# Kernel tuning notes

Hardware: AMD Instinct MI355X
Metric: run time of the kernel (lower is better)

## Reference

```python
import jax, jax.numpy as jnp
import numpy as np

N, E, B = 50000, 800000, 64
IN_DIM, HID = 128, 64
H1 = 2  # heads in gat1
NEG_SLOPE = 0.2


def _glorot(key, shape):
    fan_in = shape[0]
    return jax.random.normal(key, shape, dtype=jnp.float32) / jnp.sqrt(jnp.float32(fan_in))


def setup_inputs() -> dict:
    key = jax.random.key(0)
    ks = jax.random.split(key, 24)
    x = jax.random.normal(ks[0], (N, IN_DIM), dtype=jnp.float32)
    edge_index = jax.random.randint(ks[1], (2, E), 0, N, dtype=jnp.int64)
    batch = jnp.sort(jax.random.randint(ks[2], (N,), 0, B, dtype=jnp.int64))
    d = {
        'x': x, 'edge_index': edge_index, 'batch': batch,
        # gat1: in=128 -> heads=2, out=64 (concat -> 128)
        'w1_l': _glorot(ks[3], (IN_DIM, H1 * HID)), 'b1_l': jnp.zeros((H1 * HID,), jnp.float32),
        'w1_r': _glorot(ks[4], (IN_DIM, H1 * HID)), 'b1_r': jnp.zeros((H1 * HID,), jnp.float32),
        'att1': _glorot(ks[5], (H1, HID)), 'bias1': jnp.zeros((H1 * HID,), jnp.float32),
        # gat2: in=128 -> heads=1, out=64
        'w2_l': _glorot(ks[6], (H1 * HID, HID)), 'b2_l': jnp.zeros((HID,), jnp.float32),
        'w2_r': _glorot(ks[7], (H1 * HID, HID)), 'b2_r': jnp.zeros((HID,), jnp.float32),
        'att2': _glorot(ks[8], (1, HID)), 'bias2': jnp.zeros((HID,), jnp.float32),
        # gate_nn: Linear(64,64) -> ReLU -> Linear(64,1)
        'gate_w1': _glorot(ks[9], (HID, HID)), 'gate_b1': jnp.zeros((HID,), jnp.float32),
        'gate_w2': _glorot(ks[10], (HID, 1)), 'gate_b2': jnp.zeros((1,), jnp.float32),
        # MLP head
        'lin1_w': _glorot(ks[11], (HID, HID)), 'lin1_b': jnp.zeros((HID,), jnp.float32),
        'lin2_w': _glorot(ks[12], (HID, 1)), 'lin2_b': jnp.zeros((1,), jnp.float32),
    }
    return d


def _segment_softmax(scores, seg, num_segments):
    # scores: [E, H]; softmax over edges sharing the same seg id (per column)
    m = jax.ops.segment_max(scores, seg, num_segments=num_segments)
    m = jnp.where(jnp.isfinite(m), m, 0.0)
    ex = jnp.exp(scores - m[seg])
    s = jax.ops.segment_sum(ex, seg, num_segments=num_segments)
    return ex / (s[seg] + 1e-16)


def _gatv2(x, src, dst, w_l, b_l, w_r, b_r, att, bias, heads, out_dim, n_nodes):
    xl = (x @ w_l + b_l).reshape(n_nodes, heads, out_dim)
    xr = (x @ w_r + b_r).reshape(n_nodes, heads, out_dim)
    e = jax.nn.leaky_relu(xl[src] + xr[dst], NEG_SLOPE)      # [E,H,D]
    score = jnp.einsum('ehd,hd->eh', e, att)                  # [E,H]
    alpha = _segment_softmax(score, dst, n_nodes)             # [E,H]
    out = jax.ops.segment_sum(alpha[..., None] * xl[src], dst, num_segments=n_nodes)
    return out.reshape(n_nodes, heads * out_dim) + bias


def reference(x, edge_index, batch, w1_l, b1_l, w1_r, b1_r, att1, bias1,
              w2_l, b2_l, w2_r, b2_r, att2, bias2,
              gate_w1, gate_b1, gate_w2, gate_b2,
              lin1_w, lin1_b, lin2_w, lin2_b):
    n = x.shape[0]
    # PyG GATv2Conv default add_self_loops=True
    loop = jnp.arange(n, dtype=edge_index.dtype)
    src = jnp.concatenate([edge_index[0], loop])
    dst = jnp.concatenate([edge_index[1], loop])

    h = jax.nn.relu(_gatv2(x, src, dst, w1_l, b1_l, w1_r, b1_r, att1, bias1, H1, HID, n))
    h = jax.nn.relu(_gatv2(h, src, dst, w2_l, b2_l, w2_r, b2_r, att2, bias2, 1, HID, n))

    # GlobalAttention pool: gate = gate_nn(h); softmax over batch; weighted sum
    gate = jax.nn.relu(h @ gate_w1 + gate_b1) @ gate_w2 + gate_b2     # [N,1]
    alpha = _segment_softmax(gate, batch, B)                           # [N,1]
    pooled = jax.ops.segment_sum(alpha * h, batch, num_segments=B)     # [B,HID]

    out = jax.nn.relu(pooled @ lin1_w + lin1_b)
    out = (out @ lin2_w + lin2_b).squeeze(-1)                          # [B]
    return out
```

## Files before the change

kernel.cpp:

```cpp
#include <hip/hip_runtime.h>

typedef float v2f __attribute__((ext_vector_type(2)));
typedef float v4f __attribute__((ext_vector_type(4)));
typedef _Float16 h4 __attribute__((ext_vector_type(4)));
typedef _Float16 f16x8 __attribute__((ext_vector_type(8)));

template<int N> struct IC { static constexpr int value = N; };


__global__ void k_init(const float* __restrict__ w1_l, const float* __restrict__ w1_r,
                       const float* __restrict__ b1_l, const float* __restrict__ b1_r,
                       const float* __restrict__ w2_l, const float* __restrict__ w2_r,
                       const float* __restrict__ b2_l, const float* __restrict__ b2_r,
                       _Float16* __restrict__ wc1h, _Float16* __restrict__ wc1l,
                       _Float16* __restrict__ wc2h, _Float16* __restrict__ wc2l,
                       float* __restrict__ bc1, float* __restrict__ bc2,
                       int* __restrict__ deg, int n){
  int i = blockIdx.x*256 + threadIdx.x;
  if (i < n) deg[i] = 0;
  if (i < 256*128){
    int col = i >> 7, k = i & 127;
    float v = (col < 128) ? w1_l[k*128 + col] : w1_r[k*128 + (col - 128)];
    _Float16 h = (_Float16)v;
    wc1h[i] = h; wc1l[i] = (_Float16)(v - (float)h);
  }
  if (i < 128*128){
    int col = i >> 7, k = i & 127;
    float v = (col < 64) ? w2_l[k*64 + col] : w2_r[k*64 + (col - 64)];
    _Float16 h = (_Float16)v;
    wc2h[i] = h; wc2l[i] = (_Float16)(v - (float)h);
  }
  if (i < 256) bc1[i] = (i < 128) ? b1_l[i] : b1_r[i - 128];
  if (i < 128) bc2[i] = (i < 64)  ? b2_l[i] : b2_r[i - 64];
}

#define SCB 256

__global__ __launch_bounds__(256) void k_hist_xcd(
    const int* __restrict__ dstp, int* __restrict__ deg, int E, int n){
  int b = blockIdx.x;
  int reg = b & 7;
  int chunk = b >> 3;
  int lo = (int)((long long)reg * n >> 3);
  int hi = (int)((long long)(reg + 1) * n >> 3);
  int per = (E + SCB - 1) / SCB;
  int e0 = chunk * per;
  int e1 = min(E, e0 + per);
  for (int e = e0 + threadIdx.x; e < e1; e += 256){
    int d = dstp[e];
    if (d >= lo && d < hi) atomicAdd(&deg[d], 1);
  }
}

__global__ void k_scan1(const int* __restrict__ deg, int* __restrict__ rowptr,
                        int* __restrict__ bsum, int n){
  __shared__ int s[256];
  int i = blockIdx.x*256 + threadIdx.x;
  int v = (i < n) ? deg[i] + 1 : 0;
  s[threadIdx.x] = v;
  __syncthreads();
  for (int off = 1; off < 256; off <<= 1){
    int t = (threadIdx.x >= off) ? s[threadIdx.x - off] : 0;
    __syncthreads();
    s[threadIdx.x] += t;
    __syncthreads();
  }
  if (i < n) rowptr[i] = s[threadIdx.x] - v;
  if (threadIdx.x == 255) bsum[blockIdx.x] = s[255];
}

__global__ void k_scan2(int* bsum, int nb){
  __shared__ int s[256];
  int v = (threadIdx.x < nb) ? bsum[threadIdx.x] : 0;
  s[threadIdx.x] = v;
  __syncthreads();
  for (int off = 1; off < 256; off <<= 1){
    int t = (threadIdx.x >= off) ? s[threadIdx.x - off] : 0;
    __syncthreads();
    s[threadIdx.x] += t;
    __syncthreads();
  }
  if (threadIdx.x < nb) bsum[threadIdx.x] = s[threadIdx.x] - v;
}

__global__ void k_scan3(int* rowptr, const int* __restrict__ bsum,
                        int* __restrict__ srcs, int* __restrict__ cursor,
                        int n, int total){
  int i = blockIdx.x*256 + threadIdx.x;
  if (i < n){
    int b = rowptr[i] + bsum[blockIdx.x];
    rowptr[i] = b;
    srcs[b] = i;
    cursor[i] = b + 1;
  }
  if (i == 0) rowptr[n] = total;
}

__global__ __launch_bounds__(256) void k_scatter_xcd(
    const int* __restrict__ srcp, const int* __restrict__ dstp,
    int* __restrict__ cursor, int* __restrict__ srcs, int E, int n){
  int b = blockIdx.x;
  int reg = b & 7;
  int chunk = b >> 3;
  int lo = (int)((long long)reg * n >> 3);
  int hi = (int)((long long)(reg + 1) * n >> 3);
  int per = (E + SCB - 1) / SCB;
  int e0 = chunk * per;
  int e1 = min(E, e0 + per);
  for (int e = e0 + threadIdx.x; e < e1; e += 256){
    int d = dstp[e];
    if (d >= lo && d < hi){
      int p = atomicAdd(&cursor[d], 1);
      srcs[p] = srcp[e];
    }
  }
}


#define MBM 64
#define MBN 128
#define MBK 32

__device__ __forceinline__ int lds_idx(int row, int k){
  return row*32 + ((((k >> 3) ^ row) & 3) << 3) + (k & 7);
}

__global__ __launch_bounds__(256) void k_gemm_mfma(
    const float* __restrict__ A, const _Float16* __restrict__ Wh,
    const _Float16* __restrict__ Wl, const float* __restrict__ bias,
    _Float16* __restrict__ Cxl, float* __restrict__ Cxr,
    int M, int K, int N, int xlCols){
  __shared__ _Float16 Ah[MBM*MBK], Al[MBM*MBK];
  __shared__ _Float16 Bh[MBN*MBK], Bl[MBN*MBK];
  int bm = blockIdx.x * MBM, bn = blockIdx.y * MBN;
  int tid = threadIdx.x;
  int lane = tid & 63, wv = tid >> 6;
  v4f acc[8] = {};
  const int fragoff = (lane & 15)*32 + ((((lane >> 4) ^ lane) & 3) << 3);
  for (int k0 = 0; k0 < K; k0 += MBK){
    #pragma unroll
    for (int l = 0; l < 2; l++){
      int idx = tid + l*256;
      int r = idx >> 3, kq = (idx & 7) * 4;
      float4 v = make_float4(0.f, 0.f, 0.f, 0.f);
      if (bm + r < M) v = *(const float4*)(A + (size_t)(bm + r)*K + k0 + kq);
      _Float16 e0 = (_Float16)v.x, e1 = (_Float16)v.y,
               e2 = (_Float16)v.z, e3 = (_Float16)v.w;
      h4 hh = {e0, e1, e2, e3};
      h4 ll = {(_Float16)(v.x - (float)e0), (_Float16)(v.y - (float)e1),
               (_Float16)(v.z - (float)e2), (_Float16)(v.w - (float)e3)};
      int o = lds_idx(r, kq);
      *(h4*)(&Ah[o]) = hh;
      *(h4*)(&Al[o]) = ll;
    }
    #pragma unroll
    for (int l = 0; l < 2; l++){
      int idx = tid + l*256;
      int c = idx >> 2, kc = (idx & 3) * 8;
      size_t go = (size_t)(bn + c)*K + k0 + kc;
      int o = lds_idx(c, kc);
      *(f16x8*)(&Bh[o]) = *(const f16x8*)(Wh + go);
      *(f16x8*)(&Bl[o]) = *(const f16x8*)(Wl + go);
    }
    __syncthreads();
    f16x8 ah = *(const f16x8*)(&Ah[wv*16*32 + fragoff]);
    f16x8 al = *(const f16x8*)(&Al[wv*16*32 + fragoff]);
    #pragma unroll
    for (int t = 0; t < 8; t++){
      f16x8 bh = *(const f16x8*)(&Bh[t*16*32 + fragoff]);
      f16x8 bl = *(const f16x8*)(&Bl[t*16*32 + fragoff]);
      acc[t] = __builtin_amdgcn_mfma_f32_16x16x32_f16(ah, bh, acc[t], 0, 0, 0);
      acc[t] = __builtin_amdgcn_mfma_f32_16x16x32_f16(ah, bl, acc[t], 0, 0, 0);
      acc[t] = __builtin_amdgcn_mfma_f32_16x16x32_f16(al, bh, acc[t], 0, 0, 0);
    }
    __syncthreads();
  }
  int rbase = bm + wv*16 + (lane >> 4)*4;
  int cl = lane & 15;
  int NR = N - xlCols;
  #pragma unroll
  for (int t = 0; t < 8; t++){
    int col = bn + t*16 + cl;
    float bv = bias[col];
    bool isXl = (bn + t*16) < xlCols;
    #pragma unroll
    for (int i = 0; i < 4; i++){
      int r = rbase + i;
      if (r < M){
        float o = acc[t][i] + bv;
        if (isXl) Cxl[(size_t)r*xlCols + col] = (_Float16)o;
        else      Cxr[(size_t)r*NR + (col - xlCols)] = o;
      }
    }
  }
}


template<int CTRL>
__device__ __forceinline__ float dpp_add(float x){
  int t = __builtin_amdgcn_update_dpp(0, __float_as_int(x), CTRL, 0xf, 0xf, true);
  return x + __int_as_float(t);
}


template<int H>
__global__ __launch_bounds__(128) void k_gat_fused(
    const _Float16* __restrict__ xlh, const float* __restrict__ xr,
    const int* __restrict__ rowptr, const int* __restrict__ srcs,
    const float* __restrict__ att, const float* __restrict__ bias,
    float* __restrict__ out, int n){
  int gid = blockIdx.x * blockDim.x + threadIdx.x;
  int nd = gid >> 6, lane = gid & 63;
  if (nd >= n) return;
  constexpr int SHIFTB = (H == 2) ? 8 : 7;
  constexpr int EPI = (H == 2) ? 2 : 4;
  const int q = lane & 15;
  const int hsel = (H == 2) ? ((lane >> 4) & 1) : 0;
  const int elane = (H == 2) ? (lane >> 5) : (lane >> 4);
  const int fpos = hsel*64 + q*4;
  const unsigned foff = (unsigned)fpos * 2u;
  const char* __restrict__ xbase = (const char*)xlh;
  v4f xrv = *(const v4f*)(xr + (size_t)nd*(H*64) + fpos);
  v4f av  = *(const v4f*)(att + fpos);
  v4f acc = {0.f, 0.f, 0.f, 0.f};
  float den = 0.f;
  int s0 = rowptr[nd], s1 = rowptr[nd+1];
  for (int base = s0; base < s1; base += 64){
    int idx = base + lane;
    int sv = (idx < s1) ? srcs[idx] : 0;
    int cnt = min(64, s1 - base);
    auto batchU = [&](int i, auto Uc, bool full){
      constexpr int U = decltype(Uc)::value;
      int aidx[U];
      h4 hv[U];
      #pragma unroll
      for (int u = 0; u < U; u++)
        aidx[u] = __builtin_amdgcn_ds_bpermute((i + u*EPI + elane) << 2, sv);
      #pragma unroll
      for (int u = 0; u < U; u++)
        hv[u] = *(const h4*)(xbase + (((unsigned)aidx[u] << SHIFTB) + foff));
      #pragma unroll
      for (int u = 0; u < U; u++){
        v4f xv = {(float)hv[u].x, (float)hv[u].y, (float)hv[u].z, (float)hv[u].w};
        v4f t  = xv + xrv;
        v4f lt = __builtin_elementwise_max(t, t * 0.2f);
        v4f pr = lt * av;
        float p = (pr.x + pr.y) + (pr.z + pr.w);
        p = dpp_add<0x111>(p);
        p = dpp_add<0x112>(p);
        p = dpp_add<0x114>(p);
        p = dpp_add<0x118>(p);
        p = __int_as_float(__builtin_amdgcn_ds_swizzle(__float_as_int(p), 0x1F0));
        float ex = __expf(p);
        if (!full) ex = (elane < cnt - (i + u*EPI)) ? ex : 0.f;
        den += ex;
        acc += xv * ex;
      }
    };
    int i = 0;
    for (; i + 8*EPI <= cnt; i += 8*EPI) batchU(i, IC<8>{}, true);
    if (i + 4*EPI <= cnt){ batchU(i, IC<4>{}, true); i += 4*EPI; }
    if (i + 2*EPI <= cnt){ batchU(i, IC<2>{}, true); i += 2*EPI; }
    for (; i < cnt; i += EPI) batchU(i, IC<1>{}, i + EPI <= cnt);
  }
  if (H == 1){
    den   += __shfl_xor(den,   16, 64);
    acc.x += __shfl_xor(acc.x, 16, 64);
    acc.y += __shfl_xor(acc.y, 16, 64);
    acc.z += __shfl_xor(acc.z, 16, 64);
    acc.w += __shfl_xor(acc.w, 16, 64);
  }
  den   += __shfl_xor(den,   32, 64);
  acc.x += __shfl_xor(acc.x, 32, 64);
  acc.y += __shfl_xor(acc.y, 32, 64);
  acc.z += __shfl_xor(acc.z, 32, 64);
  acc.w += __shfl_xor(acc.w, 32, 64);
  if (lane < 16*H){
    v4f bv = *(const v4f*)(bias + fpos);
    float inv = 1.f / (den + 1e-16f);
    v4f o = acc * inv + bv;
    v4f z = {0.f, 0.f, 0.f, 0.f};
    o = __builtin_elementwise_max(o, z);
    *(v4f*)(out + (size_t)nd*(H*64) + fpos) = o;
  }
}


__global__ __launch_bounds__(256) void k_gate(
    const float* __restrict__ h2, const float* __restrict__ gw1,
    const float* __restrict__ gb1, const float* __restrict__ gw2,
    const float* __restrict__ gb2, float* __restrict__ exn, int M){
  __shared__ float As[32][64 + 4];
  __shared__ float Ws[32][64];
  int bm = blockIdx.x * 64;
  int tid = threadIdx.x;
  int tx = tid & 15, ty = tid >> 4;
  float acc[4][4] = {};
  for (int k0 = 0; k0 < 64; k0 += 32){
    #pragma unroll
    for (int l = 0; l < 2; l++){
      int idx = tid + l*256;
      int r = idx >> 3, c4 = (idx & 7) * 4;
      float4 v = make_float4(0.f, 0.f, 0.f, 0.f);
      if (bm + r < M) v = *(const float4*)(h2 + (size_t)(bm + r)*64 + k0 + c4);
      As[c4+0][r] = v.x; As[c4+1][r] = v.y; As[c4+2][r] = v.z; As[c4+3][r] = v.w;
      int kr = idx >> 4, wc4 = (idx & 15) * 4;
      *(float4*)(&Ws[kr][wc4]) = *(const float4*)(gw1 + (size_t)(k0 + kr)*64 + wc4);
    }
    __syncthreads();
    #pragma unroll
    for (int k = 0; k < 32; k++){
      float4 a4 = *(const float4*)(&As[k][ty*4]);
      float4 w4 = *(const float4*)(&Ws[k][tx*4]);
      float av[4] = {a4.x, a4.y, a4.z, a4.w};
      float wv[4] = {w4.x, w4.y, w4.z, w4.w};
      #pragma unroll
      for (int i = 0; i < 4; i++)
        #pragma unroll
        for (int j = 0; j < 4; j++)
          acc[i][j] = fmaf(av[i], wv[j], acc[i][j]);
    }
    __syncthreads();
  }
  float4 b4 = *(const float4*)(gb1 + tx*4);
  float4 w2 = *(const float4*)(gw2 + tx*4);
  float gb2v = gb2[0];
  #pragma unroll
  for (int i = 0; i < 4; i++){
    float p = fmaxf(acc[i][0] + b4.x, 0.f) * w2.x;
    p = fmaf(fmaxf(acc[i][1] + b4.y, 0.f), w2.y, p);
    p = fmaf(fmaxf(acc[i][2] + b4.z, 0.f), w2.z, p);
    p = fmaf(fmaxf(acc[i][3] + b4.w, 0.f), w2.w, p);
    p = dpp_add<0x111>(p);
    p = dpp_add<0x112>(p);
    p = dpp_add<0x114>(p);
    p = dpp_add<0x118>(p);
    if (tx == 15){
      int r = bm + ty*4 + i;
      if (r < M) exn[r] = __expf(p + gb2v);
    }
  }
}


__global__ __launch_bounds__(1024) void k_pool_mlp(
    const float* __restrict__ h2, const float* __restrict__ exn,
    const int* __restrict__ batch, int n,
    const float* __restrict__ l1w, const float* __restrict__ l1b,
    const float* __restrict__ l2w, const float* __restrict__ l2b,
    float* __restrict__ out){
  __shared__ float accs[16][64];
  __shared__ float dens[16];
  int b = blockIdx.x;
  int tid = threadIdx.x, lane = tid & 63, wv = tid >> 6;
  int lo = 0, hi = n;
  while (lo < hi){ int m = (lo + hi) >> 1; if (batch[m] < b) lo = m + 1; else hi = m; }
  int start = lo;
  hi = n;
  while (lo < hi){ int m = (lo + hi) >> 1; if (batch[m] < b + 1) lo = m + 1; else hi = m; }
  int end = lo;
  float acc = 0.f, den = 0.f;
  for (int nd = start + wv; nd < end; nd += 16){
    float ex = exn[nd];
    den += ex;
    acc = fmaf(ex, h2[(size_t)nd*64 + lane], acc);
  }
  accs[wv][lane] = acc;
  if (lane == 0) dens[wv] = den;
  __syncthreads();
  if (wv == 0){
    float p = 0.f, d = 0.f;
    #pragma unroll
    for (int w = 0; w < 16; w++){ p += accs[w][lane]; d += dens[w]; }
    p = p / (d + 1e-16f);
    float t = l1b[lane];
    #pragma unroll
    for (int k = 0; k < 64; k++)
      t = fmaf(__shfl(p, k, 64), l1w[k*64 + lane], t);
    t = fmaxf(t, 0.f) * l2w[lane];
    #pragma unroll
    for (int off = 32; off; off >>= 1) t += __shfl_xor(t, off, 64);
    if (lane == 0) out[b] = t + l2b[0];
  }
}


extern "C" void kernel_launch(void* const* d_in, const int* in_sizes, int n_in,
                              void* d_out, int out_size, void* d_ws, size_t ws_size,
                              hipStream_t stream){
  const float* x    = (const float*)d_in[0];
  const int*   ei   = (const int*)  d_in[1];
  const int*   batch= (const int*)  d_in[2];
  const float* w1_l = (const float*)d_in[3];  const float* b1_l = (const float*)d_in[4];
  const float* w1_r = (const float*)d_in[5];  const float* b1_r = (const float*)d_in[6];
  const float* att1 = (const float*)d_in[7];  const float* bias1= (const float*)d_in[8];
  const float* w2_l = (const float*)d_in[9];  const float* b2_l = (const float*)d_in[10];
  const float* w2_r = (const float*)d_in[11]; const float* b2_r = (const float*)d_in[12];
  const float* att2 = (const float*)d_in[13]; const float* bias2= (const float*)d_in[14];
  const float* gw1  = (const float*)d_in[15]; const float* gb1  = (const float*)d_in[16];
  const float* gw2  = (const float*)d_in[17]; const float* gb2  = (const float*)d_in[18];
  const float* l1w  = (const float*)d_in[19]; const float* l1b  = (const float*)d_in[20];
  const float* l2w  = (const float*)d_in[21]; const float* l2b  = (const float*)d_in[22];

  const int n = in_sizes[0] / 128;
  const int E = in_sizes[1] / 2;
  const int Bb = out_size;
  const int Etot = E + n;
  const int* srcp = ei;
  const int* dstp = ei + E;

  char* wsbase = (char*)d_ws;
  size_t off = 0;
  auto alloc = [&](size_t bytes)->char*{
    char* p = wsbase + off;
    off = (off + bytes + 255) & ~(size_t)255;
    return p;
  };
  int*   deg    = (int*)  alloc((size_t)n*4);
  int*   rowptr = (int*)  alloc((size_t)(n+1)*4);
  int*   cursor = (int*)  alloc((size_t)n*4);
  int*   bsum   = (int*)  alloc(1024);
  int*   srcs   = (int*)  alloc((size_t)Etot*4);
  _Float16* wc1h = (_Float16*)alloc(256*128*2);
  _Float16* wc1l = (_Float16*)alloc(256*128*2);
  _Float16* wc2h = (_Float16*)alloc(128*128*2);
  _Float16* wc2l = (_Float16*)alloc(128*128*2);
  float* bc1    = (float*)alloc(256*4);
  float* bc2    = (float*)alloc(128*4);
  _Float16* xlh1 = (_Float16*)alloc((size_t)n*128*2);
  float* xr1    = (float*)alloc((size_t)n*128*4);
  float* h1     = (float*)alloc((size_t)n*128*4);
  _Float16* xlh2 = xlh1;
  float* xr2 = xr1;
  float* h2  = xr1 + (size_t)n*64;
  float* exn = h1;

  int nb = (n + 255) / 256;
  int ib = (((n > 32768) ? n : 32768) + 255) / 256;

  k_init<<<ib, 256, 0, stream>>>(w1_l, w1_r, b1_l, b1_r, w2_l, w2_r, b2_l, b2_r,
                                 wc1h, wc1l, wc2h, wc2l, bc1, bc2, deg, n);
  k_hist_xcd<<<8*SCB, 256, 0, stream>>>(dstp, deg, E, n);
  k_scan1<<<nb, 256, 0, stream>>>(deg, rowptr, bsum, n);
  k_scan2<<<1, 256, 0, stream>>>(bsum, nb);
  k_scan3<<<nb, 256, 0, stream>>>(rowptr, bsum, srcs, cursor, n, Etot);
  k_scatter_xcd<<<8*SCB, 256, 0, stream>>>(srcp, dstp, cursor, srcs, E, n);

  dim3 g1((n + MBM - 1)/MBM, 2);
  k_gemm_mfma<<<g1, 256, 0, stream>>>(x, wc1h, wc1l, bc1, xlh1, xr1, n, 128, 256, 128);
  long long thr = (long long)n * 64;
  int gatb = (int)((thr + 127)/128);
  k_gat_fused<2><<<gatb, 128, 0, stream>>>(xlh1, xr1, rowptr, srcs, att1, bias1, h1, n);

  dim3 g2((n + MBM - 1)/MBM, 1);
  k_gemm_mfma<<<g2, 256, 0, stream>>>(h1, wc2h, wc2l, bc2, xlh2, xr2, n, 128, 128, 64);
  k_gat_fused<1><<<gatb, 128, 0, stream>>>(xlh2, xr2, rowptr, srcs, att2, bias2, h2, n);

  k_gate<<<(n + 63)/64, 256, 0, stream>>>(h2, gw1, gb1, gw2, gb2, exn, n);

  k_pool_mlp<<<Bb, 1024, 0, stream>>>(h2, exn, batch, n, l1w, l1b, l2w, l2b, (float*)d_out);
}
```

Baseline: 336.7 us.

## Merge weight prep with histogram and overlap edge scatter with first GEMM

Weight conversion and degree histogram are merged into one launch, with a memset replacing the kernel-based degree zeroing. The edge scatter is fused with the first-layer GEMM as a heterogeneous grid, where the first blocks do CSR scatter and the rest do GEMM tiles. The two are independent, so the GEMM can run concurrently and fill the GPU while scatter atomics are latency-bound. This removes launch gaps and serialization, but shared-memory allocation from the GEMM body now applies to the scatter blocks as well, which may lower their occupancy.

```diff
diff --git a/kernel.cpp b/kernel.cpp
--- a/kernel.cpp
+++ b/kernel.cpp
@@ -7,48 +7,51 @@
 
 template<int N> struct IC { static constexpr int value = N; };
 
-
-__global__ void k_init(const float* __restrict__ w1_l, const float* __restrict__ w1_r,
-                       const float* __restrict__ b1_l, const float* __restrict__ b1_r,
-                       const float* __restrict__ w2_l, const float* __restrict__ w2_r,
-                       const float* __restrict__ b2_l, const float* __restrict__ b2_r,
-                       _Float16* __restrict__ wc1h, _Float16* __restrict__ wc1l,
-                       _Float16* __restrict__ wc2h, _Float16* __restrict__ wc2l,
-                       float* __restrict__ bc1, float* __restrict__ bc2,
-                       int* __restrict__ deg, int n){
-  int i = blockIdx.x*256 + threadIdx.x;
-  if (i < n) deg[i] = 0;
-  if (i < 256*128){
-    int col = i >> 7, k = i & 127;
-    float v = (col < 128) ? w1_l[k*128 + col] : w1_r[k*128 + (col - 128)];
-    _Float16 h = (_Float16)v;
-    wc1h[i] = h; wc1l[i] = (_Float16)(v - (float)h);
-  }
-  if (i < 128*128){
-    int col = i >> 7, k = i & 127;
-    float v = (col < 64) ? w2_l[k*64 + col] : w2_r[k*64 + (col - 64)];
-    _Float16 h = (_Float16)v;
-    wc2h[i] = h; wc2l[i] = (_Float16)(v - (float)h);
-  }
-  if (i < 256) bc1[i] = (i < 128) ? b1_l[i] : b1_r[i - 128];
-  if (i < 128) bc2[i] = (i < 64)  ? b2_l[i] : b2_r[i - 64];
-}
-
 #define SCB 256
-
-__global__ __launch_bounds__(256) void k_hist_xcd(
+#define MBM 64
+#define MBN 128
+#define MBK 32
+
+
+__global__ __launch_bounds__(256) void k_init_hist(
+    const float* __restrict__ w1_l, const float* __restrict__ w1_r,
+    const float* __restrict__ b1_l, const float* __restrict__ b1_r,
+    const float* __restrict__ w2_l, const float* __restrict__ w2_r,
+    const float* __restrict__ b2_l, const float* __restrict__ b2_r,
+    _Float16* __restrict__ wc1h, _Float16* __restrict__ wc1l,
+    _Float16* __restrict__ wc2h, _Float16* __restrict__ wc2l,
+    float* __restrict__ bc1, float* __restrict__ bc2,
     const int* __restrict__ dstp, int* __restrict__ deg, int E, int n){
   int b = blockIdx.x;
-  int reg = b & 7;
-  int chunk = b >> 3;
-  int lo = (int)((long long)reg * n >> 3);
-  int hi = (int)((long long)(reg + 1) * n >> 3);
-  int per = (E + SCB - 1) / SCB;
-  int e0 = chunk * per;
-  int e1 = min(E, e0 + per);
-  for (int e = e0 + threadIdx.x; e < e1; e += 256){
-    int d = dstp[e];
-    if (d >= lo && d < hi) atomicAdd(&deg[d], 1);
+  if (b < 128){
+    int i = b*256 + threadIdx.x;
+    {
+      int col = i >> 7, k = i & 127;
+      float v = (col < 128) ? w1_l[k*128 + col] : w1_r[k*128 + (col - 128)];
+      _Float16 h = (_Float16)v;
+      wc1h[i] = h; wc1l[i] = (_Float16)(v - (float)h);
+    }
+    if (i < 128*128){
+      int col = i >> 7, k = i & 127;
+      float v = (col < 64) ? w2_l[k*64 + col] : w2_r[k*64 + (col - 64)];
+      _Float16 h = (_Float16)v;
+      wc2h[i] = h; wc2l[i] = (_Float16)(v - (float)h);
+    }
+    if (i < 256) bc1[i] = (i < 128) ? b1_l[i] : b1_r[i - 128];
+    if (i < 128) bc2[i] = (i < 64)  ? b2_l[i] : b2_r[i - 64];
+  } else {
+    int hb = b - 128;
+    int reg = hb & 7;
+    int chunk = hb >> 3;
+    int lo = (int)((long long)reg * n >> 3);
+    int hi = (int)((long long)(reg + 1) * n >> 3);
+    int per = (E + SCB - 1) / SCB;
+    int e0 = chunk * per;
+    int e1 = min(E, e0 + per);
+    for (int e = e0 + threadIdx.x; e < e1; e += 256){
+      int d = dstp[e];
+      if (d >= lo && d < hi) atomicAdd(&deg[d], 1);
+    }
   }
 }
 
@@ -96,43 +99,18 @@
   if (i == 0) rowptr[n] = total;
 }
 
-__global__ __launch_bounds__(256) void k_scatter_xcd(
-    const int* __restrict__ srcp, const int* __restrict__ dstp,
-    int* __restrict__ cursor, int* __restrict__ srcs, int E, int n){
-  int b = blockIdx.x;
-  int reg = b & 7;
-  int chunk = b >> 3;
-  int lo = (int)((long long)reg * n >> 3);
-  int hi = (int)((long long)(reg + 1) * n >> 3);
-  int per = (E + SCB - 1) / SCB;
-  int e0 = chunk * per;
-  int e1 = min(E, e0 + per);
-  for (int e = e0 + threadIdx.x; e < e1; e += 256){
-    int d = dstp[e];
-    if (d >= lo && d < hi){
-      int p = atomicAdd(&cursor[d], 1);
-      srcs[p] = srcp[e];
-    }
-  }
-}
-
-
-#define MBM 64
-#define MBN 128
-#define MBK 32
 
 __device__ __forceinline__ int lds_idx(int row, int k){
   return row*32 + ((((k >> 3) ^ row) & 3) << 3) + (k & 7);
 }
 
-__global__ __launch_bounds__(256) void k_gemm_mfma(
+__device__ __forceinline__ void gemm_mfma_body(
     const float* __restrict__ A, const _Float16* __restrict__ Wh,
     const _Float16* __restrict__ Wl, const float* __restrict__ bias,
     _Float16* __restrict__ Cxl, float* __restrict__ Cxr,
-    int M, int K, int N, int xlCols){
+    int M, int K, int N, int xlCols, int bm, int bn){
   __shared__ _Float16 Ah[MBM*MBK], Al[MBM*MBK];
   __shared__ _Float16 Bh[MBN*MBK], Bl[MBN*MBK];
-  int bm = blockIdx.x * MBM, bn = blockIdx.y * MBN;
   int tid = threadIdx.x;
   int lane = tid & 63, wv = tid >> 6;
   v4f acc[8] = {};
@@ -192,6 +170,47 @@
         else      Cxr[(size_t)r*NR + (col - xlCols)] = o;
       }
     }
+  }
+}
+
+__global__ __launch_bounds__(256) void k_gemm_mfma(
+    const float* __restrict__ A, const _Float16* __restrict__ Wh,
+    const _Float16* __restrict__ Wl, const float* __restrict__ bias,
+    _Float16* __restrict__ Cxl, float* __restrict__ Cxr,
+    int M, int K, int N, int xlCols){
+  gemm_mfma_body(A, Wh, Wl, bias, Cxl, Cxr, M, K, N, xlCols,
+                 blockIdx.x * MBM, blockIdx.y * MBN);
+}
+
+
+__global__ __launch_bounds__(256) void k_scatter_gemm(
+    const int* __restrict__ srcp, const int* __restrict__ dstp,
+    int* __restrict__ cursor, int* __restrict__ srcs, int E, int n,
+    const float* __restrict__ A, const _Float16* __restrict__ Wh,
+    const _Float16* __restrict__ Wl, const float* __restrict__ bias,
+    _Float16* __restrict__ Cxl, float* __restrict__ Cxr,
+    int M, int K, int N, int xlCols, int nbx){
+  int b = blockIdx.x;
+  if (b < 8*SCB){
+    int reg = b & 7;
+    int chunk = b >> 3;
+    int lo = (int)((long long)reg * n >> 3);
+    int hi = (int)((long long)(reg + 1) * n >> 3);
+    int per = (E + SCB - 1) / SCB;
+    int e0 = chunk * per;
+    int e1 = min(E, e0 + per);
+    for (int e = e0 + threadIdx.x; e < e1; e += 256){
+      int d = dstp[e];
+      if (d >= lo && d < hi){
+        int p = atomicAdd(&cursor[d], 1);
+        srcs[p] = srcp[e];
+      }
+    }
+  } else {
+    int g = b - 8*SCB;
+    int bx = g % nbx, by = g / nbx;
+    gemm_mfma_body(A, Wh, Wl, bias, Cxl, Cxr, M, K, N, xlCols,
+                   bx * MBM, by * MBN);
   }
 }
 
@@ -436,23 +455,25 @@
   float* exn = h1;
 
   int nb = (n + 255) / 256;
-  int ib = (((n > 32768) ? n : 32768) + 255) / 256;
-
-  k_init<<<ib, 256, 0, stream>>>(w1_l, w1_r, b1_l, b1_r, w2_l, w2_r, b2_l, b2_r,
-                                 wc1h, wc1l, wc2h, wc2l, bc1, bc2, deg, n);
-  k_hist_xcd<<<8*SCB, 256, 0, stream>>>(dstp, deg, E, n);
+  int nbx = (n + MBM - 1)/MBM;
+
+  hipMemsetAsync(deg, 0, (size_t)n*4, stream);
+  k_init_hist<<<128 + 8*SCB, 256, 0, stream>>>(
+      w1_l, w1_r, b1_l, b1_r, w2_l, w2_r, b2_l, b2_r,
+      wc1h, wc1l, wc2h, wc2l, bc1, bc2, dstp, deg, E, n);
   k_scan1<<<nb, 256, 0, stream>>>(deg, rowptr, bsum, n);
   k_scan2<<<1, 256, 0, stream>>>(bsum, nb);
   k_scan3<<<nb, 256, 0, stream>>>(rowptr, bsum, srcs, cursor, n, Etot);
-  k_scatter_xcd<<<8*SCB, 256, 0, stream>>>(srcp, dstp, cursor, srcs, E, n);
-
-  dim3 g1((n + MBM - 1)/MBM, 2);
-  k_gemm_mfma<<<g1, 256, 0, stream>>>(x, wc1h, wc1l, bc1, xlh1, xr1, n, 128, 256, 128);
+
+  k_scatter_gemm<<<8*SCB + nbx*2, 256, 0, stream>>>(
+      srcp, dstp, cursor, srcs, E, n,
+      x, wc1h, wc1l, bc1, xlh1, xr1, n, 128, 256, 128, nbx);
+
   long long thr = (long long)n * 64;
   int gatb = (int)((thr + 127)/128);
   k_gat_fused<2><<<gatb, 128, 0, stream>>>(xlh1, xr1, rowptr, srcs, att1, bias1, h1, n);
 
-  dim3 g2((n + MBM - 1)/MBM, 1);
+  dim3 g2(nbx, 1);
   k_gemm_mfma<<<g2, 256, 0, stream>>>(h1, wc2h, wc2l, bc2, xlh2, xr2, n, 128, 128, 64);
   k_gat_fused<1><<<gatb, 128, 0, stream>>>(xlh2, xr2, rowptr, srcs, att2, bias2, h2, n);
 
```

Result: faster. 326.5 us (median of 2 runs) (-3.0%).
